# Optimization experiments

Hardware: AMD Instinct MI355X
Metric: run time of the kernel (lower is better)

The kernel has to match this reference:

```python
import jax, jax.numpy as jnp
import numpy as np
from jax import lax

SEQ_LEN, PRED_LEN, C_IN, D_MODEL, KS = 96, 48, 7, 128, 5
PAD = (KS - 1) // 2


def setup_inputs() -> dict:
    key = jax.random.key(0)
    ks = jax.random.split(key, 20)
    B = 512
    s = 0.02
    inp = {
        "x_enc": jax.random.normal(ks[0], (B, SEQ_LEN, C_IN), jnp.float32),
        "x_mark": jax.random.randint(ks[1], (B, SEQ_LEN, 4), 0, 7),
        "y_mark": jax.random.randint(ks[2], (B, SEQ_LEN + PRED_LEN, 4), 0, 7),
        # temporal embedding tables
        "hour_emb": jax.random.normal(ks[3], (24, D_MODEL)) * s,
        "weekday_emb": jax.random.normal(ks[4], (7, D_MODEL)) * s,
        "day_emb": jax.random.normal(ks[5], (32, D_MODEL)) * s,
        "month_emb": jax.random.normal(ks[6], (13, D_MODEL)) * s,
        # value embedding Linear(C_IN -> D_MODEL)
        "W_val": jax.random.normal(ks[7], (D_MODEL, C_IN)) * s,
        "b_val": jnp.zeros((D_MODEL,)),
        # three Conv1d(D_MODEL, D_MODEL, KS)
        "conv1_w": jax.random.normal(ks[8], (D_MODEL, D_MODEL, KS)) * s,
        "conv1_b": jnp.zeros((D_MODEL,)),
        "conv2_w": jax.random.normal(ks[9], (D_MODEL, D_MODEL, KS)) * s,
        "conv2_b": jnp.zeros((D_MODEL,)),
        "conv3_w": jax.random.normal(ks[10], (D_MODEL, D_MODEL, KS)) * s,
        "conv3_b": jnp.zeros((D_MODEL,)),
        # GRU (PyTorch layout: 3*D rows ordered [r, z, n])
        "gru_Wi": jax.random.normal(ks[11], (3 * D_MODEL, D_MODEL)) * s,
        "gru_Wh": jax.random.normal(ks[12], (3 * D_MODEL, D_MODEL)) * s,
        "gru_bi": jnp.zeros((3 * D_MODEL,)),
        "gru_bh": jnp.zeros((3 * D_MODEL,)),
        # fc Linear(D_MODEL -> C_IN)
        "fc_w": jax.random.normal(ks[13], (C_IN, D_MODEL)) * s,
        "fc_b": jnp.zeros((C_IN,)),
    }
    return inp


def _conv1d(x, w, b):
    # x: [B, D, T], w: [O, I, K]
    y = lax.conv_general_dilated(x, w, window_strides=(1,), padding=[(PAD, PAD)],
                                 dimension_numbers=("NCH", "OIH", "NCH"))
    return y + b[None, :, None]


def _gru_last(x, Wi, Wh, bi, bh):
    # x: [B, T, D] -> final hidden state [B, D] (PyTorch GRU equations)
    B, T, D = x.shape
    gx = jnp.einsum("btd,gd->btg", x, Wi) + bi  # [B, T, 3D]
    h0 = jnp.zeros((B, D), x.dtype)

    def step(h, gxt):
        gh = h @ Wh.T + bh
        r = jax.nn.sigmoid(gxt[:, :D] + gh[:, :D])
        z = jax.nn.sigmoid(gxt[:, D:2 * D] + gh[:, D:2 * D])
        n = jnp.tanh(gxt[:, 2 * D:] + r * gh[:, 2 * D:])
        return (1.0 - z) * n + z * h, None

    h_last, _ = lax.scan(step, h0, jnp.swapaxes(gx, 0, 1))
    return h_last


def reference(x_enc, x_mark, y_mark,
              hour_emb, weekday_emb, day_emb, month_emb,
              W_val, b_val,
              conv1_w, conv1_b, conv2_w, conv2_b, conv3_w, conv3_b,
              gru_Wi, gru_Wh, gru_bi, gru_bh, fc_w, fc_b):
    B = x_enc.shape[0]
    # temporal embedding for the full y_mark window (pointwise; precompute once)
    temb = (hour_emb[y_mark[:, :, 0]] + weekday_emb[y_mark[:, :, 1]]
            + day_emb[y_mark[:, :, 2]] + month_emb[y_mark[:, :, 3]])  # [B, L, D]

    x_cat = jnp.concatenate([x_enc, jnp.zeros((B, PRED_LEN, C_IN), x_enc.dtype)], axis=1)

    def one_step(x_cat, i):
        xw = lax.dynamic_slice(x_cat, (0, i, 0), (B, SEQ_LEN, C_IN))
        tw = lax.dynamic_slice(temb, (0, i, 0), (B, SEQ_LEN, D_MODEL))
        x = jnp.einsum("btc,dc->btd", xw, W_val) + b_val + tw  # [B, T, D]
        x = jnp.swapaxes(x, 1, 2)  # [B, D, T]
        x = jax.nn.relu(_conv1d(x, conv1_w, conv1_b))
        x = jax.nn.relu(_conv1d(x, conv2_w, conv2_b))
        x = jax.nn.relu(_conv1d(x, conv3_w, conv3_b))
        x = jnp.swapaxes(x, 1, 2)  # [B, T, D]
        h = _gru_last(x, gru_Wi, gru_Wh, gru_bi, gru_bh)  # [B, D]
        pred = h @ fc_w.T + fc_b  # [B, C]
        x_cat = lax.dynamic_update_slice(x_cat, pred[:, None, :], (0, SEQ_LEN + i, 0))
        return x_cat, None

    x_cat, _ = lax.scan(one_step, x_cat, jnp.arange(PRED_LEN))
    return x_cat[:, -PRED_LEN:, :]
```

## Files before the change

### kernel.cpp

```cpp
#include <hip/hip_runtime.h>

#define B_SZ 512
#define SEQ 96
#define PRED 48
#define TOT 144
#define CIN 7
#define DM 128
#define GDIM 384
#define KS 5

#define CSTR 132
#define ASUB (20*CSTR)
#define WROW 136
#define SWZ(o) ((o) + ((((o) >> 6)) << 2))

#define W_CONV (KS*DM*DM)
#define OFF_WIT (3*W_CONV)
#define OFF_WHT (3*W_CONV + DM*GDIM)
#define W_TOTAL (3*W_CONV + 2*DM*GDIM)

#define NBB 2

__device__ float g_gxg[(size_t)B_SZ*TOT*GDIM];
__device__ float g_gxe[B_SZ*12*GDIM];
__device__ float g_wT[W_TOTAL];

__global__ void prep_weights(const float* __restrict__ w1, const float* __restrict__ w2,
                             const float* __restrict__ w3, const float* __restrict__ Wi,
                             const float* __restrict__ Wh) {
    int tid = blockIdx.x*256 + threadIdx.x;
    if (tid < 3*W_CONV) {
        int l = tid / W_CONV, r = tid % W_CONV;
        int o = r & 127, c = (r >> 7) & 127, k = r >> 14;
        const float* w = (l==0) ? w1 : ((l==1) ? w2 : w3);
        g_wT[tid] = w[o*(DM*KS) + c*KS + k];
    } else if (tid < W_TOTAL) {
        int r = tid - 3*W_CONV;
        int m = r / (DM*GDIM), q = r % (DM*GDIM);
        int g = q % GDIM, c = q / GDIM;
        const float* W = (m==0) ? Wi : Wh;
        g_wT[tid] = W[g*DM + c];
    }
}

template<int NJ>
__device__ __forceinline__ void fma8(float (&acc)[NJ][8], int j, float a,
                                     const float4& wA, const float4& wB) {
    acc[j][0] = fmaf(a, wA.x, acc[j][0]);
    acc[j][1] = fmaf(a, wA.y, acc[j][1]);
    acc[j][2] = fmaf(a, wA.z, acc[j][2]);
    acc[j][3] = fmaf(a, wA.w, acc[j][3]);
    acc[j][4] = fmaf(a, wB.x, acc[j][4]);
    acc[j][5] = fmaf(a, wB.y, acc[j][5]);
    acc[j][6] = fmaf(a, wB.z, acc[j][6]);
    acc[j][7] = fmaf(a, wB.w, acc[j][7]);
}

__device__ __forceinline__ void stage_conv_chunk(float* __restrict__ wbuf,
                                                 const float* __restrict__ wT,
                                                 int cc, int tid) {
    const int cj = tid >> 5, oo = (tid & 31) * 4;
    #pragma unroll
    for (int k = 0; k < KS; ++k)
        *(float4*)(wbuf + (k*8 + cj)*WROW + SWZ(oo)) =
            *(const float4*)(wT + (k*DM + cc*8 + cj)*DM + oo);
}

template<int NJ>
__device__ __forceinline__ void conv_layer_chunked(float* __restrict__ buf,
                                                   float* __restrict__ wbuf,
                                                   const float* __restrict__ wT,
                                                   const float* __restrict__ bias,
                                                   int nrow, int winO, int tid) {
    const int og = tid & 15, ttg = tid >> 4;
    const int o0 = og*8, so0 = SWZ(o0), r0 = ttg*NJ;
    const bool act = (r0 < nrow);
    float acc[NJ][8];
    #pragma unroll
    for (int u = 0; u < 8; ++u) {
        float bv = bias[o0+u];
        #pragma unroll
        for (int j = 0; j < NJ; ++j) acc[j][u] = bv;
    }
    for (int cc = 0; cc < DM/8; ++cc) {
        __syncthreads();
        stage_conv_chunk(wbuf, wT, cc, tid);
        __syncthreads();
        if (act) {
            const int c0 = cc*8;
            #pragma unroll
            for (int cj = 0; cj < 8; cj += 2) {
                float2 a2[NJ+4];
                #pragma unroll
                for (int m = 0; m < NJ+4; ++m)
                    a2[m] = *(const float2*)(buf + (r0+m)*CSTR + c0 + cj);
                #pragma unroll
                for (int k = 0; k < KS; ++k) {
                    const float4 wA0 = *(const float4*)(wbuf + (k*8+cj)*WROW + so0);
                    const float4 wB0 = *(const float4*)(wbuf + (k*8+cj)*WROW + so0 + 4);
                    const float4 wA1 = *(const float4*)(wbuf + (k*8+cj+1)*WROW + so0);
                    const float4 wB1 = *(const float4*)(wbuf + (k*8+cj+1)*WROW + so0 + 4);
                    #pragma unroll
                    for (int j = 0; j < NJ; ++j) {
                        fma8(acc, j, a2[j+k].x, wA0, wB0);
                        fma8(acc, j, a2[j+k].y, wA1, wB1);
                    }
                }
            }
        }
    }
    __syncthreads();
    if (act) {
        #pragma unroll
        for (int j = 0; j < NJ; ++j) {
            int q = r0 + j, w = winO + q;
            bool valid = (w >= 0) && (w < SEQ);
            #pragma unroll
            for (int u = 0; u < 8; ++u)
                buf[q*CSTR + o0+u] = valid ? fmaxf(acc[j][u], 0.f) : 0.f;
        }
    }
    __syncthreads();
}

__launch_bounds__(256, 3)
__global__ void init_kernel(const float* __restrict__ x_enc,
                            const int* __restrict__ y_mark,
                            const float* __restrict__ hour_e, const float* __restrict__ wk_e,
                            const float* __restrict__ day_e, const float* __restrict__ mon_e,
                            const float* __restrict__ W_val, const float* __restrict__ b_val,
                            const float* __restrict__ b1, const float* __restrict__ b2,
                            const float* __restrict__ b3, const float* __restrict__ gbi) {
    __shared__ float buf[60*CSTR];
    __shared__ float wbuf[KS*8*WROW];
    const int tid = threadIdx.x;
    const int b = blockIdx.x;
    const int cs = blockIdx.y * 48;

    for (int e = tid; e < 60*DM; e += 256) {
        int q = e >> 7, d = e & 127;
        int w = cs - 6 + q;
        float v = 0.f;
        if (w >= 0 && w < SEQ) {
            const float* xr = x_enc + (b*SEQ + w)*CIN;
            v = b_val[d];
            #pragma unroll
            for (int c = 0; c < CIN; ++c) v = fmaf(xr[c], W_val[d*CIN + c], v);
            const int* ym = y_mark + (b*TOT + w)*4;
            v += hour_e[ym[0]*DM + d] + wk_e[ym[1]*DM + d]
               + day_e[ym[2]*DM + d] + mon_e[ym[3]*DM + d];
        }
        buf[q*CSTR + d] = v;
    }
    conv_layer_chunked<4>(buf, wbuf, g_wT,            b1, 56, cs - 4, tid);
    conv_layer_chunked<4>(buf, wbuf, g_wT + W_CONV,   b2, 52, cs - 2, tid);
    conv_layer_chunked<3>(buf, wbuf, g_wT + 2*W_CONV, b3, 48, cs,     tid);

    const int og = tid & 15, ttg = tid >> 4;
    const int g0 = og*24, r0 = ttg*3;
    const float* WiT = g_wT + OFF_WIT;
    float ga[3][24];
    #pragma unroll
    for (int e = 0; e < 24; ++e) {
        float bv = gbi[g0+e];
        #pragma unroll
        for (int j = 0; j < 3; ++j) ga[j][e] = bv;
    }
    for (int cc = 0; cc < DM/8; ++cc) {
        __syncthreads();
        #pragma unroll
        for (int s = 0; s < 3; ++s)
            ((float4*)wbuf)[s*256 + tid] = ((const float4*)(WiT + cc*8*GDIM))[s*256 + tid];
        __syncthreads();
        const int c0 = cc*8;
        #pragma unroll
        for (int cj = 0; cj < 8; cj += 2) {
            float2 a2[3];
            #pragma unroll
            for (int m = 0; m < 3; ++m)
                a2[m] = *(const float2*)(buf + (r0+m)*CSTR + c0 + cj);
            float4 w4[6];
            #pragma unroll
            for (int q = 0; q < 6; ++q)
                w4[q] = *(const float4*)(wbuf + cj*GDIM + g0 + q*4);
            const float* wv = (const float*)w4;
            #pragma unroll
            for (int j = 0; j < 3; ++j)
                #pragma unroll
                for (int e = 0; e < 24; ++e)
                    ga[j][e] = fmaf(a2[j].x, wv[e], ga[j][e]);
            #pragma unroll
            for (int q = 0; q < 6; ++q)
                w4[q] = *(const float4*)(wbuf + (cj+1)*GDIM + g0 + q*4);
            #pragma unroll
            for (int j = 0; j < 3; ++j)
                #pragma unroll
                for (int e = 0; e < 24; ++e)
                    ga[j][e] = fmaf(a2[j].y, wv[e], ga[j][e]);
        }
    }
    #pragma unroll
    for (int j = 0; j < 3; ++j) {
        int w = cs + r0 + j;
        if (w >= 6 && w < 90) {
            float* gxo = g_gxg + ((size_t)b*TOT + w)*GDIM + g0;
            #pragma unroll
            for (int q = 0; q < 6; ++q)
                *(float4*)(gxo + q*4) = *(const float4*)&ga[j][q*4];
        }
    }
}

template<int NJ>
__device__ __forceinline__ void mlayer(float* __restrict__ abuf, float* __restrict__ wbuf,
                                       const float* __restrict__ wT,
                                       const float* __restrict__ bias,
                                       int R, int off, int tid) {
    const int og = tid & 15, ttg = tid >> 4;
    const int o0 = og*8, so0 = SWZ(o0);
    const int m0 = ttg * NJ;
    const bool act = (m0 < 2*R);
    int s = 0, r0 = 0;
    if (act) { s = m0 / R; r0 = m0 - s*R; }
    float* in = abuf + s*ASUB;
    float acc[NJ][8];
    #pragma unroll
    for (int u = 0; u < 8; ++u) {
        float bv = bias[o0+u];
        #pragma unroll
        for (int j = 0; j < NJ; ++j) acc[j][u] = bv;
    }
    for (int cc = 0; cc < DM/8; ++cc) {
        __syncthreads();
        stage_conv_chunk(wbuf, wT, cc, tid);
        __syncthreads();
        if (act) {
            const int c0 = cc*8;
            #pragma unroll
            for (int cj = 0; cj < 8; cj += 2) {
                float2 a2[NJ+4];
                #pragma unroll
                for (int m = 0; m < NJ+4; ++m)
                    a2[m] = *(const float2*)(in + (r0+m)*CSTR + c0 + cj);
                #pragma unroll
                for (int k = 0; k < KS; ++k) {
                    const float4 wA0 = *(const float4*)(wbuf + (k*8+cj)*WROW + so0);
                    const float4 wB0 = *(const float4*)(wbuf + (k*8+cj)*WROW + so0 + 4);
                    const float4 wA1 = *(const float4*)(wbuf + (k*8+cj+1)*WROW + so0);
                    const float4 wB1 = *(const float4*)(wbuf + (k*8+cj+1)*WROW + so0 + 4);
                    #pragma unroll
                    for (int j = 0; j < NJ; ++j) {
                        fma8(acc, j, a2[j+k].x, wA0, wB0);
                        fma8(acc, j, a2[j+k].y, wA1, wB1);
                    }
                }
            }
        }
    }
    __syncthreads();
    if (act) {
        const int wb = s ? 83 : -6;
        #pragma unroll
        for (int j = 0; j < NJ; ++j) {
            int q = r0 + j, w = wb + off + q;
            bool valid = (w >= 0) && (w < SEQ);
            #pragma unroll
            for (int u = 0; u < 8; ++u)
                in[q*CSTR + o0+u] = valid ? fmaxf(acc[j][u], 0.f) : 0.f;
        }
    }
    __syncthreads();
}

__launch_bounds__(256, 3)
__global__ void step_kernel(int i, const float* __restrict__ x_enc,
                            const int* __restrict__ y_mark,
                            const float* __restrict__ hour_e, const float* __restrict__ wk_e,
                            const float* __restrict__ day_e, const float* __restrict__ mon_e,
                            const float* __restrict__ W_val, const float* __restrict__ b_val,
                            const float* __restrict__ b1, const float* __restrict__ b2,
                            const float* __restrict__ b3, const float* __restrict__ gbi,
                            const float* __restrict__ out) {
    __shared__ float abuf[2*ASUB];
    __shared__ float wbuf[16*GDIM];
    const int tid = threadIdx.x;
    const int b = blockIdx.x;

    for (int e = tid; e < 2*20*DM; e += 256) {
        int s = e / (20*DM);
        int rem = e - s*(20*DM);
        int q = rem >> 7, d = rem & 127;
        int wb = s ? 83 : -6;
        int w = wb + q;
        float v = 0.f;
        if (w >= 0 && w < SEQ) {
            int p = i + w;
            const float* xr = (p < SEQ) ? (x_enc + (b*SEQ + p)*CIN)
                                        : (out + (b*PRED + (p - SEQ))*CIN);
            v = b_val[d];
            #pragma unroll
            for (int c = 0; c < CIN; ++c) v = fmaf(xr[c], W_val[d*CIN + c], v);
            const int* ym = y_mark + (b*TOT + p)*4;
            v += hour_e[ym[0]*DM + d] + wk_e[ym[1]*DM + d]
               + day_e[ym[2]*DM + d] + mon_e[ym[3]*DM + d];
        }
        abuf[s*ASUB + q*CSTR + d] = v;
    }
    mlayer<2>(abuf, wbuf, g_wT,            b1, 16, 2, tid);
    mlayer<2>(abuf, wbuf, g_wT + W_CONV,   b2, 12, 4, tid);
    mlayer<1>(abuf, wbuf, g_wT + 2*W_CONV, b3,  8, 6, tid);

    const int mp = tid >> 5;
    const int g0 = (tid & 31) * 12;
    const int s = mp >> 2;
    const int row0 = (2*mp) & 7;
    const float* a0p = abuf + s*ASUB + row0*CSTR;
    const float* a1p = a0p + CSTR;
    const float* WiT = g_wT + OFF_WIT;
    float ga[2][12];
    #pragma unroll
    for (int e = 0; e < 12; ++e) { float bv = gbi[g0+e]; ga[0][e] = bv; ga[1][e] = bv; }
    for (int cc = 0; cc < 8; ++cc) {
        __syncthreads();
        for (int x = tid; x < 16*GDIM/4; x += 256)
            ((float4*)wbuf)[x] = ((const float4*)(WiT + cc*16*GDIM))[x];
        __syncthreads();
        #pragma unroll
        for (int c = 0; c < 16; ++c) {
            float av0 = a0p[cc*16 + c];
            float av1 = a1p[cc*16 + c];
            const float* wr = wbuf + c*GDIM + g0;
            #pragma unroll
            for (int q4 = 0; q4 < 3; ++q4) {
                float4 w4 = *(const float4*)(wr + q4*4);
                ga[0][q4*4+0] = fmaf(av0, w4.x, ga[0][q4*4+0]);
                ga[0][q4*4+1] = fmaf(av0, w4.y, ga[0][q4*4+1]);
                ga[0][q4*4+2] = fmaf(av0, w4.z, ga[0][q4*4+2]);
                ga[0][q4*4+3] = fmaf(av0, w4.w, ga[0][q4*4+3]);
                ga[1][q4*4+0] = fmaf(av1, w4.x, ga[1][q4*4+0]);
                ga[1][q4*4+1] = fmaf(av1, w4.y, ga[1][q4*4+1]);
                ga[1][q4*4+2] = fmaf(av1, w4.z, ga[1][q4*4+2]);
                ga[1][q4*4+3] = fmaf(av1, w4.w, ga[1][q4*4+3]);
            }
        }
    }
    const int wb = s ? 83 : -6;
    #pragma unroll
    for (int j = 0; j < 2; ++j) {
        int w = wb + 6 + row0 + j;
        float* dst = nullptr;
        if (s == 0) {
            if (w < 6) dst = g_gxe + ((size_t)b*12 + w)*GDIM + g0;
        } else {
            if (w == 89)      dst = g_gxg + ((size_t)b*TOT + (i + 89))*GDIM + g0;
            else if (w < SEQ) dst = g_gxe + ((size_t)b*12 + (w - 84))*GDIM + g0;
        }
        if (dst) {
            *(float4*)(dst)     = *(const float4*)&ga[j][0];
            *(float4*)(dst + 4) = *(const float4*)&ga[j][4];
            *(float4*)(dst + 8) = *(const float4*)&ga[j][8];
        }
    }
}

__launch_bounds__(512, 2)
__global__ void gru_rec(int i, const float* __restrict__ gbh,
                        const float* __restrict__ fc_w, const float* __restrict__ fc_b,
                        float* __restrict__ out) {
    __shared__ __align__(16) float H[2][NBB][DM];
    __shared__ float P[3][4][NBB][DM];
    const int tid = threadIdx.x;
    const int j = tid & 127, s = tid >> 7;
    const int b0 = blockIdx.x * NBB;

    float whr[32], whz[32], whn[32];
    {
        const float* Wp = g_wT + OFF_WHT + (size_t)(32*s)*GDIM + j;
        #pragma unroll
        for (int c = 0; c < 32; ++c) {
            whr[c] = Wp[c*GDIM];
            whz[c] = Wp[c*GDIM + DM];
            whn[c] = Wp[c*GDIM + 2*DM];
        }
    }

    const int cb = s & 1, cj = j;
    const bool comb = (tid < NBB*DM);
    float bhr = 0.f, bhz = 0.f, bhn = 0.f;
    if (comb) {
        bhr = gbh[cj]; bhz = gbh[DM + cj]; bhn = gbh[2*DM + cj];
        H[0][cb][cj] = 0.f;
    }

    const float* gxg_b0 = g_gxg + (size_t)(b0)*TOT*GDIM;
    const float* gxe_b0 = g_gxe + (size_t)(b0)*12*GDIM;
    auto gp = [&](int t, int bb) -> const float* {
        return (t < 6)  ? (gxe_b0 + (size_t)bb*12*GDIM + t*GDIM)
             : (t < 90) ? (gxg_b0 + (size_t)bb*TOT*GDIM + (size_t)(i + t)*GDIM)
                        : (gxe_b0 + (size_t)bb*12*GDIM + (t - 84)*GDIM);
    };

    float gxr = 0.f, gxz = 0.f, gxn = 0.f;
    if (comb) {
        const float* g0p = gp(0, cb);
        gxr = g0p[cj]; gxz = g0p[DM + cj]; gxn = g0p[2*DM + cj];
    }
    __syncthreads();

    for (int t = 0; t < SEQ; ++t) {
        #pragma unroll
        for (int b = 0; b < NBB; ++b) {
            const float* Hc = &H[t & 1][b][32*s];
            float ar = 0.f, az = 0.f, an = 0.f;
            #pragma unroll
            for (int c = 0; c < 32; c += 4) {
                float4 h4 = *(const float4*)(Hc + c);
                ar = fmaf(h4.x, whr[c],   ar); az = fmaf(h4.x, whz[c],   az); an = fmaf(h4.x, whn[c],   an);
                ar = fmaf(h4.y, whr[c+1], ar); az = fmaf(h4.y, whz[c+1], az); an = fmaf(h4.y, whn[c+1], an);
                ar = fmaf(h4.z, whr[c+2], ar); az = fmaf(h4.z, whz[c+2], az); an = fmaf(h4.z, whn[c+2], an);
                ar = fmaf(h4.w, whr[c+3], ar); az = fmaf(h4.w, whz[c+3], az); an = fmaf(h4.w, whn[c+3], an);
            }
            P[0][s][b][j] = ar;
            P[1][s][b][j] = az;
            P[2][s][b][j] = an;
        }
        __syncthreads();
        if (comb) {
            float ar = bhr + ((P[0][0][cb][cj] + P[0][1][cb][cj]) + (P[0][2][cb][cj] + P[0][3][cb][cj]));
            float az = bhz + ((P[1][0][cb][cj] + P[1][1][cb][cj]) + (P[1][2][cb][cj] + P[1][3][cb][cj]));
            float an = bhn + ((P[2][0][cb][cj] + P[2][1][cb][cj]) + (P[2][2][cb][cj] + P[2][3][cb][cj]));
            float r = 1.f/(1.f + __expf(-(gxr + ar)));
            float z = 1.f/(1.f + __expf(-(gxz + az)));
            float xn = gxn + r*an;
            float e2 = __expf(2.f*xn);
            float n = 1.f - 2.f/(e2 + 1.f);
            float h = (1.f - z)*n + z*H[t & 1][cb][cj];
            H[(t + 1) & 1][cb][cj] = h;
            if (t + 1 < SEQ) {
                const float* gq = gp(t + 1, cb);
                gxr = gq[cj]; gxz = gq[DM + cj]; gxn = gq[2*DM + cj];
            }
        }
        __syncthreads();
    }

    if (tid < NBB*CIN) {
        int bb = tid / CIN, o = tid % CIN;
        float p = fc_b[o];
        const float* Hf = H[0][bb];
        #pragma unroll
        for (int d = 0; d < DM; ++d) p = fmaf(fc_w[o*DM + d], Hf[d], p);
        out[((b0 + bb)*PRED + i)*CIN + o] = p;
    }
}

extern "C" void kernel_launch(void* const* d_in, const int* in_sizes, int n_in,
                              void* d_out, int out_size, void* d_ws, size_t ws_size,
                              hipStream_t stream) {
    const float* x_enc  = (const float*)d_in[0];
    const int*   y_mark = (const int*)d_in[2];
    const float* hour_e = (const float*)d_in[3];
    const float* wk_e   = (const float*)d_in[4];
    const float* day_e  = (const float*)d_in[5];
    const float* mon_e  = (const float*)d_in[6];
    const float* W_val  = (const float*)d_in[7];
    const float* b_val  = (const float*)d_in[8];
    const float* c1w    = (const float*)d_in[9];
    const float* c1b    = (const float*)d_in[10];
    const float* c2w    = (const float*)d_in[11];
    const float* c2b    = (const float*)d_in[12];
    const float* c3w    = (const float*)d_in[13];
    const float* c3b    = (const float*)d_in[14];
    const float* Wi     = (const float*)d_in[15];
    const float* Wh     = (const float*)d_in[16];
    const float* gbi    = (const float*)d_in[17];
    const float* gbh    = (const float*)d_in[18];
    const float* fcw    = (const float*)d_in[19];
    const float* fcb    = (const float*)d_in[20];
    float* out = (float*)d_out;

    prep_weights<<<(W_TOTAL + 255)/256, 256, 0, stream>>>(c1w, c2w, c3w, Wi, Wh);

    init_kernel<<<dim3(B_SZ, 2), 256, 0, stream>>>(x_enc, y_mark,
        hour_e, wk_e, day_e, mon_e, W_val, b_val, c1b, c2b, c3b, gbi);

    for (int i = 0; i < PRED; ++i) {
        step_kernel<<<B_SZ, 256, 0, stream>>>(i, x_enc, y_mark,
            hour_e, wk_e, day_e, mon_e, W_val, b_val, c1b, c2b, c3b, gbi, out);
        gru_rec<<<B_SZ/NBB, 512, 0, stream>>>(i, gbh, fcw, fcb, out);
    }
}
```

Measured before the change: 11.28 ms.

## Fuse per-step conv/input-projection kernel with GRU recurrence kernel

Merges step_kernel and gru_rec into one 512-thread kernel that handles two batch rows per block. The edge-window GRU input projections stay in shared memory instead of making a global round trip, and one launch per step is removed. The hidden state is also kept in a register. The tradeoff is half as many blocks, more shared memory per block, and a waves_per_eu limit of 2, so occupancy and parallelism across the grid drop.

```diff
diff --git a/kernel.cpp b/kernel.cpp
--- a/kernel.cpp
+++ b/kernel.cpp
@@ -22,7 +22,6 @@
 #define NBB 2
 
 __device__ float g_gxg[(size_t)B_SZ*TOT*GDIM];
-__device__ float g_gxe[B_SZ*12*GDIM];
 __device__ float g_wT[W_TOTAL];
 
 __global__ void prep_weights(const float* __restrict__ w1, const float* __restrict__ w2,
@@ -219,7 +218,7 @@
     const int og = tid & 15, ttg = tid >> 4;
     const int o0 = og*8, so0 = SWZ(o0);
     const int m0 = ttg * NJ;
-    const bool act = (m0 < 2*R);
+    const bool act = (m0 < 4*R);
     int s = 0, r0 = 0;
     if (act) { s = m0 / R; r0 = m0 - s*R; }
     float* in = abuf + s*ASUB;
@@ -232,7 +231,11 @@
     }
     for (int cc = 0; cc < DM/8; ++cc) {
         __syncthreads();
-        stage_conv_chunk(wbuf, wT, cc, tid);
+        for (int x = tid; x < 1280; x += 512) {
+            int k = x >> 8, rr = (x >> 5) & 7, oo = (x & 31)*4;
+            *(float4*)(wbuf + (k*8+rr)*WROW + SWZ(oo)) =
+                *(const float4*)(wT + (k*DM + cc*8 + rr)*DM + oo);
+        }
         __syncthreads();
         if (act) {
             const int c0 = cc*8;
@@ -259,7 +262,7 @@
     }
     __syncthreads();
     if (act) {
-        const int wb = s ? 83 : -6;
+        const int wb = (s & 1) ? 83 : -6;
         #pragma unroll
         for (int j = 0; j < NJ; ++j) {
             int q = r0 + j, w = wb + off + q;
@@ -272,25 +275,29 @@
     __syncthreads();
 }
 
-__launch_bounds__(256, 3)
-__global__ void step_kernel(int i, const float* __restrict__ x_enc,
-                            const int* __restrict__ y_mark,
-                            const float* __restrict__ hour_e, const float* __restrict__ wk_e,
-                            const float* __restrict__ day_e, const float* __restrict__ mon_e,
-                            const float* __restrict__ W_val, const float* __restrict__ b_val,
-                            const float* __restrict__ b1, const float* __restrict__ b2,
-                            const float* __restrict__ b3, const float* __restrict__ gbi,
-                            const float* __restrict__ out) {
-    __shared__ float abuf[2*ASUB];
+__global__ __attribute__((amdgpu_waves_per_eu(2, 2)))
+__launch_bounds__(512)
+void step_gru(int i, const float* __restrict__ x_enc,
+              const int* __restrict__ y_mark,
+              const float* __restrict__ hour_e, const float* __restrict__ wk_e,
+              const float* __restrict__ day_e, const float* __restrict__ mon_e,
+              const float* __restrict__ W_val, const float* __restrict__ b_val,
+              const float* __restrict__ b1, const float* __restrict__ b2,
+              const float* __restrict__ b3, const float* __restrict__ gbi,
+              const float* __restrict__ gbh, const float* __restrict__ fc_w,
+              const float* __restrict__ fc_b, float* __restrict__ out) {
+    __shared__ float abuf[4*ASUB];
     __shared__ float wbuf[16*GDIM];
+    __shared__ float gxe[NBB*12*GDIM];
     const int tid = threadIdx.x;
-    const int b = blockIdx.x;
-
-    for (int e = tid; e < 2*20*DM; e += 256) {
+    const int b0 = blockIdx.x * NBB;
+
+    for (int e = tid; e < 4*20*DM; e += 512) {
         int s = e / (20*DM);
         int rem = e - s*(20*DM);
         int q = rem >> 7, d = rem & 127;
-        int wb = s ? 83 : -6;
+        int wb = (s & 1) ? 83 : -6;
+        int b = b0 + (s >> 1);
         int w = wb + q;
         float v = 0.f;
         if (w >= 0 && w < SEQ) {
@@ -310,72 +317,68 @@
     mlayer<2>(abuf, wbuf, g_wT + W_CONV,   b2, 12, 4, tid);
     mlayer<1>(abuf, wbuf, g_wT + 2*W_CONV, b3,  8, 6, tid);
 
-    const int mp = tid >> 5;
-    const int g0 = (tid & 31) * 12;
-    const int s = mp >> 2;
-    const int row0 = (2*mp) & 7;
-    const float* a0p = abuf + s*ASUB + row0*CSTR;
-    const float* a1p = a0p + CSTR;
-    const float* WiT = g_wT + OFF_WIT;
-    float ga[2][12];
-    #pragma unroll
-    for (int e = 0; e < 12; ++e) { float bv = gbi[g0+e]; ga[0][e] = bv; ga[1][e] = bv; }
-    for (int cc = 0; cc < 8; ++cc) {
-        __syncthreads();
-        for (int x = tid; x < 16*GDIM/4; x += 256)
-            ((float4*)wbuf)[x] = ((const float4*)(WiT + cc*16*GDIM))[x];
-        __syncthreads();
-        #pragma unroll
-        for (int c = 0; c < 16; ++c) {
-            float av0 = a0p[cc*16 + c];
-            float av1 = a1p[cc*16 + c];
-            const float* wr = wbuf + c*GDIM + g0;
-            #pragma unroll
-            for (int q4 = 0; q4 < 3; ++q4) {
-                float4 w4 = *(const float4*)(wr + q4*4);
-                ga[0][q4*4+0] = fmaf(av0, w4.x, ga[0][q4*4+0]);
-                ga[0][q4*4+1] = fmaf(av0, w4.y, ga[0][q4*4+1]);
-                ga[0][q4*4+2] = fmaf(av0, w4.z, ga[0][q4*4+2]);
-                ga[0][q4*4+3] = fmaf(av0, w4.w, ga[0][q4*4+3]);
-                ga[1][q4*4+0] = fmaf(av1, w4.x, ga[1][q4*4+0]);
-                ga[1][q4*4+1] = fmaf(av1, w4.y, ga[1][q4*4+1]);
-                ga[1][q4*4+2] = fmaf(av1, w4.z, ga[1][q4*4+2]);
-                ga[1][q4*4+3] = fmaf(av1, w4.w, ga[1][q4*4+3]);
-            }
-        }
-    }
-    const int wb = s ? 83 : -6;
-    #pragma unroll
-    for (int j = 0; j < 2; ++j) {
-        int w = wb + 6 + row0 + j;
-        float* dst = nullptr;
-        if (s == 0) {
-            if (w < 6) dst = g_gxe + ((size_t)b*12 + w)*GDIM + g0;
-        } else {
-            if (w == 89)      dst = g_gxg + ((size_t)b*TOT + (i + 89))*GDIM + g0;
-            else if (w < SEQ) dst = g_gxe + ((size_t)b*12 + (w - 84))*GDIM + g0;
-        }
-        if (dst) {
-            *(float4*)(dst)     = *(const float4*)&ga[j][0];
-            *(float4*)(dst + 4) = *(const float4*)&ga[j][4];
-            *(float4*)(dst + 8) = *(const float4*)&ga[j][8];
-        }
-    }
-}
-
-__launch_bounds__(512, 2)
-__global__ void gru_rec(int i, const float* __restrict__ gbh,
-                        const float* __restrict__ fc_w, const float* __restrict__ fc_b,
-                        float* __restrict__ out) {
-    __shared__ __align__(16) float H[2][NBB][DM];
-    __shared__ float P[3][4][NBB][DM];
-    const int tid = threadIdx.x;
-    const int j = tid & 127, s = tid >> 7;
-    const int b0 = blockIdx.x * NBB;
-
+    {
+        const int mp = tid >> 5;
+        const int g0 = (tid & 31) * 12;
+        const int s = mp >> 2;
+        const int row0 = (2*mp) & 7;
+        const float* a0p = abuf + s*ASUB + row0*CSTR;
+        const float* a1p = a0p + CSTR;
+        const float* WiT = g_wT + OFF_WIT;
+        float ga[2][12];
+        #pragma unroll
+        for (int e = 0; e < 12; ++e) { float bv = gbi[g0+e]; ga[0][e] = bv; ga[1][e] = bv; }
+        for (int cc = 0; cc < 8; ++cc) {
+            __syncthreads();
+            for (int x = tid; x < 16*GDIM/4; x += 512)
+                ((float4*)wbuf)[x] = ((const float4*)(WiT + cc*16*GDIM))[x];
+            __syncthreads();
+            #pragma unroll
+            for (int c = 0; c < 16; ++c) {
+                float av0 = a0p[cc*16 + c];
+                float av1 = a1p[cc*16 + c];
+                const float* wr = wbuf + c*GDIM + g0;
+                #pragma unroll
+                for (int q4 = 0; q4 < 3; ++q4) {
+                    float4 w4 = *(const float4*)(wr + q4*4);
+                    ga[0][q4*4+0] = fmaf(av0, w4.x, ga[0][q4*4+0]);
+                    ga[0][q4*4+1] = fmaf(av0, w4.y, ga[0][q4*4+1]);
+                    ga[0][q4*4+2] = fmaf(av0, w4.z, ga[0][q4*4+2]);
+                    ga[0][q4*4+3] = fmaf(av0, w4.w, ga[0][q4*4+3]);
+                    ga[1][q4*4+0] = fmaf(av1, w4.x, ga[1][q4*4+0]);
+                    ga[1][q4*4+1] = fmaf(av1, w4.y, ga[1][q4*4+1]);
+                    ga[1][q4*4+2] = fmaf(av1, w4.z, ga[1][q4*4+2]);
+                    ga[1][q4*4+3] = fmaf(av1, w4.w, ga[1][q4*4+3]);
+                }
+            }
+        }
+        const int bb = s >> 1, edge = s & 1;
+        const int b = b0 + bb;
+        #pragma unroll
+        for (int j = 0; j < 2; ++j) {
+            int w = (edge ? 83 : -6) + 6 + row0 + j;
+            float* dst = nullptr;
+            if (edge == 0) {
+                if (w < 6) dst = gxe + ((size_t)bb*12 + w)*GDIM + g0;
+            } else {
+                if (w == 89)      dst = g_gxg + ((size_t)b*TOT + (i + 89))*GDIM + g0;
+                else if (w < SEQ) dst = gxe + ((size_t)bb*12 + (w - 84))*GDIM + g0;
+            }
+            if (dst) {
+                *(float4*)(dst)     = *(const float4*)&ga[j][0];
+                *(float4*)(dst + 4) = *(const float4*)&ga[j][4];
+                *(float4*)(dst + 8) = *(const float4*)&ga[j][8];
+            }
+        }
+    }
+    __syncthreads();
+
+    float* P = wbuf;
+    float* H = wbuf + 3*4*NBB*DM;
+    const int j = tid & 127, s4 = tid >> 7;
     float whr[32], whz[32], whn[32];
     {
-        const float* Wp = g_wT + OFF_WHT + (size_t)(32*s)*GDIM + j;
+        const float* Wp = g_wT + OFF_WHT + (size_t)(32*s4)*GDIM + j;
         #pragma unroll
         for (int c = 0; c < 32; ++c) {
             whr[c] = Wp[c*GDIM];
@@ -383,34 +386,23 @@
             whn[c] = Wp[c*GDIM + 2*DM];
         }
     }
-
-    const int cb = s & 1, cj = j;
     const bool comb = (tid < NBB*DM);
-    float bhr = 0.f, bhz = 0.f, bhn = 0.f;
+    const int cb = s4 & 1, cj = j;
+    float bhr = 0.f, bhz = 0.f, bhn = 0.f, h = 0.f;
+    float gxr = 0.f, gxz = 0.f, gxn = 0.f;
     if (comb) {
         bhr = gbh[cj]; bhz = gbh[DM + cj]; bhn = gbh[2*DM + cj];
-        H[0][cb][cj] = 0.f;
-    }
-
-    const float* gxg_b0 = g_gxg + (size_t)(b0)*TOT*GDIM;
-    const float* gxe_b0 = g_gxe + (size_t)(b0)*12*GDIM;
-    auto gp = [&](int t, int bb) -> const float* {
-        return (t < 6)  ? (gxe_b0 + (size_t)bb*12*GDIM + t*GDIM)
-             : (t < 90) ? (gxg_b0 + (size_t)bb*TOT*GDIM + (size_t)(i + t)*GDIM)
-                        : (gxe_b0 + (size_t)bb*12*GDIM + (t - 84)*GDIM);
-    };
-
-    float gxr = 0.f, gxz = 0.f, gxn = 0.f;
-    if (comb) {
-        const float* g0p = gp(0, cb);
-        gxr = g0p[cj]; gxz = g0p[DM + cj]; gxn = g0p[2*DM + cj];
+        H[(0*NBB + cb)*DM + cj] = 0.f;
+        gxr = gxe[(size_t)cb*12*GDIM + cj];
+        gxz = gxe[(size_t)cb*12*GDIM + DM + cj];
+        gxn = gxe[(size_t)cb*12*GDIM + 2*DM + cj];
     }
     __syncthreads();
 
     for (int t = 0; t < SEQ; ++t) {
         #pragma unroll
-        for (int b = 0; b < NBB; ++b) {
-            const float* Hc = &H[t & 1][b][32*s];
+        for (int bb = 0; bb < NBB; ++bb) {
+            const float* Hc = H + (((t & 1)*NBB) + bb)*DM + 32*s4;
             float ar = 0.f, az = 0.f, an = 0.f;
             #pragma unroll
             for (int c = 0; c < 32; c += 4) {
@@ -420,24 +412,31 @@
                 ar = fmaf(h4.z, whr[c+2], ar); az = fmaf(h4.z, whz[c+2], az); an = fmaf(h4.z, whn[c+2], an);
                 ar = fmaf(h4.w, whr[c+3], ar); az = fmaf(h4.w, whz[c+3], az); an = fmaf(h4.w, whn[c+3], an);
             }
-            P[0][s][b][j] = ar;
-            P[1][s][b][j] = az;
-            P[2][s][b][j] = an;
+            P[((0*4 + s4)*NBB + bb)*DM + j] = ar;
+            P[((1*4 + s4)*NBB + bb)*DM + j] = az;
+            P[((2*4 + s4)*NBB + bb)*DM + j] = an;
         }
         __syncthreads();
         if (comb) {
-            float ar = bhr + ((P[0][0][cb][cj] + P[0][1][cb][cj]) + (P[0][2][cb][cj] + P[0][3][cb][cj]));
-            float az = bhz + ((P[1][0][cb][cj] + P[1][1][cb][cj]) + (P[1][2][cb][cj] + P[1][3][cb][cj]));
-            float an = bhn + ((P[2][0][cb][cj] + P[2][1][cb][cj]) + (P[2][2][cb][cj] + P[2][3][cb][cj]));
-            float r = 1.f/(1.f + __expf(-(gxr + ar)));
-            float z = 1.f/(1.f + __expf(-(gxz + az)));
-            float xn = gxn + r*an;
+            float ar2 = bhr, az2 = bhz, an2 = bhn;
+            #pragma unroll
+            for (int ss = 0; ss < 4; ++ss) {
+                ar2 += P[((0*4 + ss)*NBB + cb)*DM + cj];
+                az2 += P[((1*4 + ss)*NBB + cb)*DM + cj];
+                an2 += P[((2*4 + ss)*NBB + cb)*DM + cj];
+            }
+            float r = 1.f/(1.f + __expf(-(gxr + ar2)));
+            float z = 1.f/(1.f + __expf(-(gxz + az2)));
+            float xn = gxn + r*an2;
             float e2 = __expf(2.f*xn);
             float n = 1.f - 2.f/(e2 + 1.f);
-            float h = (1.f - z)*n + z*H[t & 1][cb][cj];
-            H[(t + 1) & 1][cb][cj] = h;
+            h = (1.f - z)*n + z*h;
+            H[(((t + 1) & 1)*NBB + cb)*DM + cj] = h;
             if (t + 1 < SEQ) {
-                const float* gq = gp(t + 1, cb);
+                int t1 = t + 1;
+                const float* gq = (t1 < 6)  ? (gxe + ((size_t)cb*12 + t1)*GDIM)
+                                : (t1 < 90) ? (g_gxg + (((size_t)(b0 + cb)*TOT) + i + t1)*GDIM)
+                                            : (gxe + ((size_t)cb*12 + (t1 - 84))*GDIM);
                 gxr = gq[cj]; gxz = gq[DM + cj]; gxn = gq[2*DM + cj];
             }
         }
@@ -447,7 +446,7 @@
     if (tid < NBB*CIN) {
         int bb = tid / CIN, o = tid % CIN;
         float p = fc_b[o];
-        const float* Hf = H[0][bb];
+        const float* Hf = H + bb*DM;
         #pragma unroll
         for (int d = 0; d < DM; ++d) p = fmaf(fc_w[o*DM + d], Hf[d], p);
         out[((b0 + bb)*PRED + i)*CIN + o] = p;
@@ -485,8 +484,8 @@
         hour_e, wk_e, day_e, mon_e, W_val, b_val, c1b, c2b, c3b, gbi);
 
     for (int i = 0; i < PRED; ++i) {
-        step_kernel<<<B_SZ, 256, 0, stream>>>(i, x_enc, y_mark,
-            hour_e, wk_e, day_e, mon_e, W_val, b_val, c1b, c2b, c3b, gbi, out);
-        gru_rec<<<B_SZ/NBB, 512, 0, stream>>>(i, gbh, fcw, fcb, out);
-    }
-}
+        step_gru<<<B_SZ/NBB, 512, 0, stream>>>(i, x_enc, y_mark,
+            hour_e, wk_e, day_e, mon_e, W_val, b_val, c1b, c2b, c3b,
+            gbi, gbh, fcw, fcb, out);
+    }
+}
```

New measurement: 12.40 ms. 9.9% more time.
